# Kernel tuning notes

Measured on AMD Instinct MI355X. Metric: run time of the kernel, lower is better.

## Reference

```python
import jax, jax.numpy as jnp
import numpy as np

DIM = 64
POS_HID = 64
ATTN_HID = DIM * 4  # attn_mlp_hidden_mult = 4
B, N = 4, 512


def setup_inputs() -> dict:
    key = jax.random.key(0)
    ks = jax.random.split(key, 12)
    s = lambda fan_in: 1.0 / np.sqrt(fan_in)
    return {
        "x": jax.random.normal(ks[0], (B, N, DIM), dtype=jnp.float32),
        "pos": jax.random.normal(ks[1], (B, N, 3), dtype=jnp.float32),
        # to_qkv: Linear(dim, 3*dim, bias=False); stored as [in, out]
        "w_qkv": jax.random.uniform(ks[2], (DIM, 3 * DIM), jnp.float32, -s(DIM), s(DIM)),
        # pos_mlp: Linear(3, POS_HID) -> ReLU -> Linear(POS_HID, dim)
        "pos_w1": jax.random.uniform(ks[3], (3, POS_HID), jnp.float32, -s(3), s(3)),
        "pos_b1": jax.random.uniform(ks[4], (POS_HID,), jnp.float32, -s(3), s(3)),
        "pos_w2": jax.random.uniform(ks[5], (POS_HID, DIM), jnp.float32, -s(POS_HID), s(POS_HID)),
        "pos_b2": jax.random.uniform(ks[6], (DIM,), jnp.float32, -s(POS_HID), s(POS_HID)),
        # attn_mlp: Linear(dim, ATTN_HID) -> ReLU -> Linear(ATTN_HID, 1)
        "attn_w1": jax.random.uniform(ks[7], (DIM, ATTN_HID), jnp.float32, -s(DIM), s(DIM)),
        "attn_b1": jax.random.uniform(ks[8], (ATTN_HID,), jnp.float32, -s(DIM), s(DIM)),
        "attn_w2": jax.random.uniform(ks[9], (ATTN_HID, 1), jnp.float32, -s(ATTN_HID), s(ATTN_HID)),
        "attn_b2": jax.random.uniform(ks[10], (1,), jnp.float32, -s(ATTN_HID), s(ATTN_HID)),
    }


def reference(x, pos, w_qkv, pos_w1, pos_b1, pos_w2, pos_b2,
              attn_w1, attn_b1, attn_w2, attn_b2):
    # qkv projection: [b,n,3d] -> q,k,v each [b,n,d]
    qkv = x @ w_qkv
    q, k, v = jnp.split(qkv, 3, axis=-1)
    # pairwise relative positions: [b,n,n,3]
    rel_pos = pos[:, :, None, :] - pos[:, None, :, :]
    # pos_mlp: [b,n,n,d]
    rel_pos_emb = jax.nn.relu(rel_pos @ pos_w1 + pos_b1) @ pos_w2 + pos_b2
    # pairwise q-k differences: [b,n,n,d]
    qk_rel = q[:, :, None, :] - k[:, None, :, :]
    # attn_mlp -> scalar sim per pair: [b,n,n]
    h = qk_rel + rel_pos_emb
    sim = (jax.nn.relu(h @ attn_w1 + attn_b1) @ attn_w2 + attn_b2)[..., 0]
    attn = jax.nn.softmax(sim, axis=-1)
    # values augmented by positional embedding, weighted sum over j
    v_aug = v[:, None, :, :] + rel_pos_emb  # [b,n,n,d]
    agg = jnp.einsum('bij,bijd->bid', attn, v_aug)
    return agg
```

## Files before the change

### kernel.cpp

```cpp
#include <hip/hip_runtime.h>
#include <hip/hip_bf16.h>
#include <stdint.h>

#define DIM 64
#define TH  256
#define NN  512
#define IB  4

typedef __attribute__((ext_vector_type(8))) short bf16x8;
typedef __attribute__((ext_vector_type(4))) float f32x4;

__device__ __forceinline__ short f2bf(float f) {
    union { float f; uint32_t u; } v; v.f = f;
    uint32_t r = v.u + 0x7fffu + ((v.u >> 16) & 1u);
    return (short)(r >> 16);
}

__global__ void prep_all(const float* __restrict__ x, const float* __restrict__ w_qkv,
                         const float* __restrict__ attn_w1,
                         const float* __restrict__ pos_w2, const float* __restrict__ pos_b2,
                         const float* __restrict__ attn_b1,
                         float* __restrict__ V, float* __restrict__ QW1, short* __restrict__ Kneg,
                         short* __restrict__ Bg, float* __restrict__ cbg) {
    const int tid = threadIdx.x;
    if (blockIdx.x >= 256) {
        const int t = (blockIdx.x - 256) * 32 + (tid >> 3);
        const int h0 = (tid & 7) * 8;
        float m[8] = {};
        for (int d = 0; d < DIM; d++) {
            float wa1 = attn_w1[d * TH + t];
            #pragma unroll
            for (int hh = 0; hh < 8; hh++) m[hh] += pos_w2[(h0 + hh) * DIM + d] * wa1;
        }
        #pragma unroll
        for (int hh = 0; hh < 8; hh++) {
            Bg[t * 128 + h0 + hh] = f2bf(m[hh]);
            Bg[t * 128 + 64 + h0 + hh] = f2bf(attn_w1[(h0 + hh) * TH + t]);
        }
        if ((tid & 7) == 0) {
            float cb = attn_b1[t];
            for (int d = 0; d < DIM; d++) cb += pos_b2[d] * attn_w1[d * TH + t];
            cbg[t] = cb;
        }
        return;
    }
    const int b = blockIdx.x >> 6, j0 = (blockIdx.x & 63) * 8;
    __shared__ float xs[8][DIM], qs[8][DIM];
    #pragma unroll
    for (int p = 0; p < 2; p++) {
        int idx = tid + p * 256;
        xs[idx >> 6][idx & 63] = x[(size_t)(b * NN + j0) * DIM + idx];
    }
    __syncthreads();
    if (tid < 192) {
        float acc[8] = {};
        for (int e = 0; e < DIM; e++) {
            float wq = w_qkv[e * 192 + tid];
            #pragma unroll
            for (int jj = 0; jj < 8; jj++) acc[jj] += xs[jj][e] * wq;
        }
        #pragma unroll
        for (int jj = 0; jj < 8; jj++) {
            size_t row = (size_t)(b * NN + j0 + jj) * DIM;
            if (tid < 64)       qs[jj][tid] = acc[jj];
            else if (tid < 128) Kneg[row + (tid - 64)] = f2bf(-acc[jj]);
            else                V[row + (tid - 128)] = acc[jj];
        }
    }
    __syncthreads();
    float aq[8] = {};
    for (int d = 0; d < DIM; d++) {
        float w = attn_w1[d * TH + tid];
        #pragma unroll
        for (int jj = 0; jj < 8; jj++) aq[jj] += qs[jj][d] * w;
    }
    #pragma unroll
    for (int jj = 0; jj < 8; jj++)
        QW1[(size_t)(b * NN + j0 + jj) * TH + tid] = aq[jj];
}

__launch_bounds__(512, 2)
__global__ void ptl_main(const float* __restrict__ pos, const float* __restrict__ pos_w1,
                         const float* __restrict__ pos_b1, const float* __restrict__ pos_w2,
                         const float* __restrict__ pos_b2, const float* __restrict__ attn_w2,
                         const float* __restrict__ V, const float* __restrict__ QW1,
                         const short* __restrict__ Kneg, const short* __restrict__ Bg,
                         const float* __restrict__ cbg, float* __restrict__ out) {
    const int b = blockIdx.x >> 7, i0 = (blockIdx.x & 127) * IB;
    const int tid = threadIdx.x;
    const int wv = tid >> 6, lane = tid & 63;
    const int lhi = lane >> 4, llo = lane & 15;

    __shared__ __align__(16) short Blds[128 * 128];
    __shared__ float posl[NN][3];
    __shared__ float2 qwl[IB][TH];
    __shared__ float4 pw4[DIM];
    __shared__ float simbuf[IB][NN];
    __shared__ float aggw[8][IB][2][DIM];
    __shared__ float fin[IB][2][DIM];
    __shared__ float wred[2][IB][8];

    for (int idx = tid; idx < NN * 3; idx += 512)
        ((float*)posl)[idx] = pos[b * NN * 3 + idx];
    if (tid < TH) {
        float w2 = attn_w2[tid], cb = cbg[tid];
        #pragma unroll
        for (int ii = 0; ii < IB; ii++) {
            float2 q2; q2.x = QW1[(size_t)(b * NN + i0 + ii) * TH + tid] + cb; q2.y = w2;
            qwl[ii][tid] = q2;
        }
    }
    if (tid < DIM) {
        float4 w; w.x = pos_w1[tid]; w.y = pos_w1[DIM + tid];
        w.z = pos_w1[2 * DIM + tid]; w.w = pos_b1[tid];
        pw4[tid] = w;
    }
    bf16x8 knf[4][2];
    #pragma unroll
    for (int jt = 0; jt < 4; jt++) {
        size_t row = (size_t)(b * NN + wv * 64 + jt * 16 + llo) * DIM;
        knf[jt][0] = *(const bf16x8*)(Kneg + row + lhi * 8);
        knf[jt][1] = *(const bf16x8*)(Kneg + row + 32 + lhi * 8);
    }
    __syncthreads();

    const char* mb = (const char*)Blds + llo * 256;
    const int s0 = ((0  + lhi) ^ llo) << 4;
    const int s1 = ((4  + lhi) ^ llo) << 4;
    const int s2 = ((8  + lhi) ^ llo) << 4;
    const int s3 = ((12 + lhi) ^ llo) << 4;

    #pragma unroll 1
    for (int half = 0; half < 2; half++) {
        if (half) __syncthreads();
        for (int idx = tid; idx < 128 * 16; idx += 512) {
            int t = idx >> 4, s = idx & 15;
            *(uint4*)((char*)Blds + t * 256 + ((s ^ (t & 15)) << 4)) =
                *(const uint4*)((const char*)Bg + ((size_t)half * 2048 + idx) * 16);
        }
        __syncthreads();

        #pragma unroll 1
        for (int ii = 0; ii < IB; ii++) {
            const float pi0 = posl[i0 + ii][0], pi1 = posl[i0 + ii][1], pi2 = posl[i0 + ii][2];
            bf16x8 gfr[4][2];
            #pragma unroll
            for (int jt = 0; jt < 4; jt++) {
                const int jA = wv * 64 + jt * 16 + llo;
                const float r0 = pi0 - posl[jA][0], r1 = pi1 - posl[jA][1], r2 = pi2 - posl[jA][2];
                #pragma unroll
                for (int kk = 0; kk < 2; kk++) {
                    #pragma unroll
                    for (int e2 = 0; e2 < 4; e2++) {
                        float4 wA = pw4[kk * 32 + lhi * 8 + 2 * e2];
                        float4 wB = pw4[kk * 32 + lhi * 8 + 2 * e2 + 1];
                        float2 p2;
                        p2.x = fmaxf(r0 * wA.x + r1 * wA.y + r2 * wA.z + wA.w, 0.f);
                        p2.y = fmaxf(r0 * wB.x + r1 * wB.y + r2 * wB.z + wB.w, 0.f);
                        union { __hip_bfloat162 h2; uint32_t u; } cv;
                        cv.h2 = __float22bfloat162_rn(p2);
                        ((uint32_t*)&gfr[jt][kk])[e2] = cv.u;
                    }
                }
            }
            float sa[4][4] = {};
            #pragma unroll 4
            for (int tt = 0; tt < 8; tt++) {
                const int t = half * 128 + tt * 16 + llo;
                bf16x8 bf0 = *(const bf16x8*)(mb + tt * 4096 + s0);
                bf16x8 bf1 = *(const bf16x8*)(mb + tt * 4096 + s1);
                bf16x8 bf2 = *(const bf16x8*)(mb + tt * 4096 + s2);
                bf16x8 bf3 = *(const bf16x8*)(mb + tt * 4096 + s3);
                const float2 qw = qwl[ii][t];
                #pragma unroll
                for (int jt = 0; jt < 4; jt++) {
                    f32x4 acc = {0.f, 0.f, 0.f, 0.f};
                    acc = __builtin_amdgcn_mfma_f32_16x16x32_bf16(gfr[jt][0], bf0, acc, 0, 0, 0);
                    acc = __builtin_amdgcn_mfma_f32_16x16x32_bf16(gfr[jt][1], bf1, acc, 0, 0, 0);
                    acc = __builtin_amdgcn_mfma_f32_16x16x32_bf16(knf[jt][0], bf2, acc, 0, 0, 0);
                    acc = __builtin_amdgcn_mfma_f32_16x16x32_bf16(knf[jt][1], bf3, acc, 0, 0, 0);
                    #pragma unroll
                    for (int r = 0; r < 4; r++)
                        sa[jt][r] += fmaxf(acc[r] + qw.x, 0.f) * qw.y;
                }
            }
            #pragma unroll
            for (int jt = 0; jt < 4; jt++) {
                #pragma unroll
                for (int r = 0; r < 4; r++) {
                    float v = sa[jt][r];
                    v += __shfl_xor(v, 1); v += __shfl_xor(v, 2);
                    v += __shfl_xor(v, 4); v += __shfl_xor(v, 8);
                    if (llo == 0) {
                        const int j = wv * 64 + jt * 16 + lhi * 4 + r;
                        if (half == 0) simbuf[ii][j] = v;
                        else           simbuf[ii][j] += v;
                    }
                }
            }
        }
    }
    __syncthreads();

    float sv[IB];
    #pragma unroll
    for (int ii = 0; ii < IB; ii++) {
        float s = simbuf[ii][tid];
        sv[ii] = s;
        float mx = s;
        #pragma unroll
        for (int off = 1; off < 64; off <<= 1) mx = fmaxf(mx, __shfl_xor(mx, off));
        if (lane == 0) wred[0][ii][wv] = mx;
    }
    __syncthreads();
    float pv[IB];
    #pragma unroll
    for (int ii = 0; ii < IB; ii++) {
        float bm = wred[0][ii][0];
        #pragma unroll
        for (int w = 1; w < 8; w++) bm = fmaxf(bm, wred[0][ii][w]);
        float p = __expf(sv[ii] - bm);
        pv[ii] = p;
        float ps = p;
        #pragma unroll
        for (int off = 1; off < 64; off <<= 1) ps += __shfl_xor(ps, off);
        if (lane == 0) wred[1][ii][wv] = ps;
    }
    __syncthreads();
    #pragma unroll
    for (int ii = 0; ii < IB; ii++) {
        float den = 0.f;
        #pragma unroll
        for (int w = 0; w < 8; w++) den += wred[1][ii][w];
        simbuf[ii][tid] = pv[ii] / den;
    }
    __syncthreads();

    {
        const int d = lane;
        const float4 wd = pw4[d];
        float pia[IB][3];
        #pragma unroll
        for (int ii = 0; ii < IB; ii++) {
            pia[ii][0] = posl[i0 + ii][0]; pia[ii][1] = posl[i0 + ii][1]; pia[ii][2] = posl[i0 + ii][2];
        }
        float av[IB] = {}, ag[IB] = {};
        const float* vb = V + (size_t)(b * NN + wv * 64) * DIM + d;
        #pragma unroll 4
        for (int jj = 0; jj < 64; jj++) {
            const int j = wv * 64 + jj;
            const float vv = vb[jj * DIM];
            const float p0 = posl[j][0], p1 = posl[j][1], p2 = posl[j][2];
            #pragma unroll
            for (int ii = 0; ii < IB; ii++) {
                const float a = simbuf[ii][j];
                av[ii] += a * vv;
                float g = (pia[ii][0] - p0) * wd.x + (pia[ii][1] - p1) * wd.y +
                          (pia[ii][2] - p2) * wd.z + wd.w;
                ag[ii] += a * fmaxf(g, 0.f);
            }
        }
        #pragma unroll
        for (int ii = 0; ii < IB; ii++) {
            aggw[wv][ii][0][d] = av[ii];
            aggw[wv][ii][1][d] = ag[ii];
        }
    }
    __syncthreads();
    {
        const int ii = tid >> 7, pp = (tid >> 6) & 1, d2 = tid & 63;
        float s = 0.f;
        #pragma unroll
        for (int w = 0; w < 8; w++) s += aggw[w][ii][pp][d2];
        fin[ii][pp][d2] = s;
    }
    __syncthreads();
    if (tid < IB * DIM) {
        const int ii = tid >> 6, d2 = tid & 63;
        float o = fin[ii][0][d2] + pos_b2[d2];
        for (int h = 0; h < DIM; h++) o += fin[ii][1][h] * pos_w2[h * DIM + d2];
        out[(size_t)(b * NN + i0 + ii) * DIM + d2] = o;
    }
}

extern "C" void kernel_launch(void* const* d_in, const int* in_sizes, int n_in,
                              void* d_out, int out_size, void* d_ws, size_t ws_size,
                              hipStream_t stream) {
    const float* x       = (const float*)d_in[0];
    const float* pos     = (const float*)d_in[1];
    const float* w_qkv   = (const float*)d_in[2];
    const float* pos_w1  = (const float*)d_in[3];
    const float* pos_b1  = (const float*)d_in[4];
    const float* pos_w2  = (const float*)d_in[5];
    const float* pos_b2  = (const float*)d_in[6];
    const float* attn_w1 = (const float*)d_in[7];
    const float* attn_b1 = (const float*)d_in[8];
    const float* attn_w2 = (const float*)d_in[9];

    char* ws = (char*)d_ws;
    short* Bg   = (short*)(ws + 0);
    float* cbg  = (float*)(ws + 65536);
    float* Vw   = (float*)(ws + 66560);
    float* QW1  = (float*)(ws + 590848);
    short* Kneg = (short*)(ws + 2688000);

    float* outp = (float*)d_out;

    prep_all<<<264, 256, 0, stream>>>(x, w_qkv, attn_w1, pos_w2, pos_b2, attn_b1,
                                      Vw, QW1, Kneg, Bg, cbg);
    ptl_main<<<4 * (NN / IB), 512, 0, stream>>>(pos, pos_w1, pos_b1, pos_w2, pos_b2,
                                                attn_w2, Vw, QW1, Kneg, Bg, cbg, outp);
}
```

Measured before the change: 234.3 us.

## Use 1024-thread blocks with 8 query rows and full resident attn_w1 tile

Doubles the query rows per block to 8 and the block size to 1024 threads, so each wave handles 32 key columns instead of 64. The full 256-wide hidden weight tile is kept in LDS, loaded once, which removes the two-pass half loop and its extra barriers. Softmax and the aggregation are restructured for 16 waves, with the aggregation done in two groups of four rows. LDS use roughly doubles and the grid halves to 256 blocks, which may reduce occupancy or leave CUs idle.

```diff
diff --git a/kernel.cpp b/kernel.cpp
--- a/kernel.cpp
+++ b/kernel.cpp
@@ -5,7 +5,7 @@
 #define DIM 64
 #define TH  256
 #define NN  512
-#define IB  4
+#define IB  8
 
 typedef __attribute__((ext_vector_type(8))) short bf16x8;
 typedef __attribute__((ext_vector_type(4))) float f32x4;
@@ -79,46 +79,57 @@
         QW1[(size_t)(b * NN + j0 + jj) * TH + tid] = aq[jj];
 }
 
-__launch_bounds__(512, 2)
+__launch_bounds__(1024, 4)
 __global__ void ptl_main(const float* __restrict__ pos, const float* __restrict__ pos_w1,
                          const float* __restrict__ pos_b1, const float* __restrict__ pos_w2,
                          const float* __restrict__ pos_b2, const float* __restrict__ attn_w2,
                          const float* __restrict__ V, const float* __restrict__ QW1,
                          const short* __restrict__ Kneg, const short* __restrict__ Bg,
                          const float* __restrict__ cbg, float* __restrict__ out) {
-    const int b = blockIdx.x >> 7, i0 = (blockIdx.x & 127) * IB;
+    const int b = blockIdx.x >> 6, i0 = (blockIdx.x & 63) * IB;
     const int tid = threadIdx.x;
     const int wv = tid >> 6, lane = tid & 63;
     const int lhi = lane >> 4, llo = lane & 15;
 
-    __shared__ __align__(16) short Blds[128 * 128];
+    __shared__ __align__(16) short Blds[TH * 128];
     __shared__ float posl[NN][3];
     __shared__ float2 qwl[IB][TH];
     __shared__ float4 pw4[DIM];
     __shared__ float simbuf[IB][NN];
-    __shared__ float aggw[8][IB][2][DIM];
+    __shared__ float aggw[16][4][2][DIM];
     __shared__ float fin[IB][2][DIM];
     __shared__ float wred[2][IB][8];
 
-    for (int idx = tid; idx < NN * 3; idx += 512)
-        ((float*)posl)[idx] = pos[b * NN * 3 + idx];
-    if (tid < TH) {
-        float w2 = attn_w2[tid], cb = cbg[tid];
-        #pragma unroll
-        for (int ii = 0; ii < IB; ii++) {
-            float2 q2; q2.x = QW1[(size_t)(b * NN + i0 + ii) * TH + tid] + cb; q2.y = w2;
-            qwl[ii][tid] = q2;
-        }
+    #pragma unroll
+    for (int p = 0; p < 4; p++) {
+        int idx = tid + p * 1024;
+        int t = idx >> 4, s = idx & 15;
+        *(uint4*)((char*)Blds + t * 256 + ((s ^ (t & 15)) << 4)) =
+            *(const uint4*)((const char*)Bg + (size_t)idx * 16);
+    }
+    #pragma unroll
+    for (int p = 0; p < 2; p++) {
+        int idx = tid + p * 1024;
+        if (idx < NN * 3) ((float*)posl)[idx] = pos[b * NN * 3 + idx];
+    }
+    #pragma unroll
+    for (int p = 0; p < 2; p++) {
+        int idx = tid + p * 1024;
+        int ii = idx >> 8, t = idx & 255;
+        float2 q2;
+        q2.x = QW1[(size_t)(b * NN + i0 + ii) * TH + t] + cbg[t];
+        q2.y = attn_w2[t];
+        qwl[ii][t] = q2;
     }
     if (tid < DIM) {
         float4 w; w.x = pos_w1[tid]; w.y = pos_w1[DIM + tid];
         w.z = pos_w1[2 * DIM + tid]; w.w = pos_b1[tid];
         pw4[tid] = w;
     }
-    bf16x8 knf[4][2];
-    #pragma unroll
-    for (int jt = 0; jt < 4; jt++) {
-        size_t row = (size_t)(b * NN + wv * 64 + jt * 16 + llo) * DIM;
+    bf16x8 knf[2][2];
+    #pragma unroll
+    for (int jt = 0; jt < 2; jt++) {
+        size_t row = (size_t)(b * NN + wv * 32 + jt * 16 + llo) * DIM;
         knf[jt][0] = *(const bf16x8*)(Kneg + row + lhi * 8);
         knf[jt][1] = *(const bf16x8*)(Kneg + row + 32 + lhi * 8);
     }
@@ -131,148 +142,136 @@
     const int s3 = ((12 + lhi) ^ llo) << 4;
 
     #pragma unroll 1
-    for (int half = 0; half < 2; half++) {
-        if (half) __syncthreads();
-        for (int idx = tid; idx < 128 * 16; idx += 512) {
-            int t = idx >> 4, s = idx & 15;
-            *(uint4*)((char*)Blds + t * 256 + ((s ^ (t & 15)) << 4)) =
-                *(const uint4*)((const char*)Bg + ((size_t)half * 2048 + idx) * 16);
+    for (int ii = 0; ii < IB; ii++) {
+        const float pi0 = posl[i0 + ii][0], pi1 = posl[i0 + ii][1], pi2 = posl[i0 + ii][2];
+        bf16x8 gfr[2][2];
+        #pragma unroll
+        for (int jt = 0; jt < 2; jt++) {
+            const int jA = wv * 32 + jt * 16 + llo;
+            const float r0 = pi0 - posl[jA][0], r1 = pi1 - posl[jA][1], r2 = pi2 - posl[jA][2];
+            #pragma unroll
+            for (int kk = 0; kk < 2; kk++) {
+                #pragma unroll
+                for (int e2 = 0; e2 < 4; e2++) {
+                    float4 wA = pw4[kk * 32 + lhi * 8 + 2 * e2];
+                    float4 wB = pw4[kk * 32 + lhi * 8 + 2 * e2 + 1];
+                    float2 p2;
+                    p2.x = fmaxf(r0 * wA.x + r1 * wA.y + r2 * wA.z + wA.w, 0.f);
+                    p2.y = fmaxf(r0 * wB.x + r1 * wB.y + r2 * wB.z + wB.w, 0.f);
+                    union { __hip_bfloat162 h2; uint32_t u; } cv;
+                    cv.h2 = __float22bfloat162_rn(p2);
+                    ((uint32_t*)&gfr[jt][kk])[e2] = cv.u;
+                }
+            }
+        }
+        float sa[2][4] = {};
+        #pragma unroll 4
+        for (int tt = 0; tt < 16; tt++) {
+            const int t = tt * 16 + llo;
+            bf16x8 bf0 = *(const bf16x8*)(mb + tt * 4096 + s0);
+            bf16x8 bf1 = *(const bf16x8*)(mb + tt * 4096 + s1);
+            bf16x8 bf2 = *(const bf16x8*)(mb + tt * 4096 + s2);
+            bf16x8 bf3 = *(const bf16x8*)(mb + tt * 4096 + s3);
+            const float2 qw = qwl[ii][t];
+            #pragma unroll
+            for (int jt = 0; jt < 2; jt++) {
+                f32x4 acc = {0.f, 0.f, 0.f, 0.f};
+                acc = __builtin_amdgcn_mfma_f32_16x16x32_bf16(gfr[jt][0], bf0, acc, 0, 0, 0);
+                acc = __builtin_amdgcn_mfma_f32_16x16x32_bf16(gfr[jt][1], bf1, acc, 0, 0, 0);
+                acc = __builtin_amdgcn_mfma_f32_16x16x32_bf16(knf[jt][0], bf2, acc, 0, 0, 0);
+                acc = __builtin_amdgcn_mfma_f32_16x16x32_bf16(knf[jt][1], bf3, acc, 0, 0, 0);
+                #pragma unroll
+                for (int r = 0; r < 4; r++)
+                    sa[jt][r] += fmaxf(acc[r] + qw.x, 0.f) * qw.y;
+            }
+        }
+        #pragma unroll
+        for (int jt = 0; jt < 2; jt++) {
+            #pragma unroll
+            for (int r = 0; r < 4; r++) {
+                float v = sa[jt][r];
+                v += __shfl_xor(v, 1); v += __shfl_xor(v, 2);
+                v += __shfl_xor(v, 4); v += __shfl_xor(v, 8);
+                if (llo == 0) simbuf[ii][wv * 32 + jt * 16 + lhi * 4 + r] = v;
+            }
+        }
+    }
+    __syncthreads();
+
+    const int iig = wv >> 3, w8 = wv & 7, j = tid & 511;
+    float sv[4], pv[4];
+    #pragma unroll
+    for (int c = 0; c < 4; c++) {
+        const int ii = 2 * c + iig;
+        float s = simbuf[ii][j];
+        sv[c] = s;
+        float mx = s;
+        #pragma unroll
+        for (int off = 1; off < 64; off <<= 1) mx = fmaxf(mx, __shfl_xor(mx, off));
+        if (lane == 0) wred[0][ii][w8] = mx;
+    }
+    __syncthreads();
+    #pragma unroll
+    for (int c = 0; c < 4; c++) {
+        const int ii = 2 * c + iig;
+        float bm = wred[0][ii][0];
+        #pragma unroll
+        for (int w = 1; w < 8; w++) bm = fmaxf(bm, wred[0][ii][w]);
+        float p = __expf(sv[c] - bm);
+        pv[c] = p;
+        float ps = p;
+        #pragma unroll
+        for (int off = 1; off < 64; off <<= 1) ps += __shfl_xor(ps, off);
+        if (lane == 0) wred[1][ii][w8] = ps;
+    }
+    __syncthreads();
+    #pragma unroll
+    for (int c = 0; c < 4; c++) {
+        const int ii = 2 * c + iig;
+        float den = 0.f;
+        #pragma unroll
+        for (int w = 0; w < 8; w++) den += wred[1][ii][w];
+        simbuf[ii][j] = pv[c] / den;
+    }
+    __syncthreads();
+
+    #pragma unroll 1
+    for (int g = 0; g < 2; g++) {
+        if (g) __syncthreads();
+        {
+            const int d = lane;
+            const float4 wd = pw4[d];
+            float av[4] = {}, ag[4] = {};
+            const float* vb = V + (size_t)(b * NN + wv * 32) * DIM + d;
+            #pragma unroll 4
+            for (int jj = 0; jj < 32; jj++) {
+                const int jx = wv * 32 + jj;
+                const float vv = vb[jj * DIM];
+                const float p0 = posl[jx][0], p1 = posl[jx][1], p2 = posl[jx][2];
+                #pragma unroll
+                for (int c = 0; c < 4; c++) {
+                    const int ii = g * 4 + c;
+                    const float a = simbuf[ii][jx];
+                    av[c] += a * vv;
+                    float gg = (posl[i0 + ii][0] - p0) * wd.x + (posl[i0 + ii][1] - p1) * wd.y +
+                               (posl[i0 + ii][2] - p2) * wd.z + wd.w;
+                    ag[c] += a * fmaxf(gg, 0.f);
+                }
+            }
+            #pragma unroll
+            for (int c = 0; c < 4; c++) {
+                aggw[wv][c][0][d] = av[c];
+                aggw[wv][c][1][d] = ag[c];
+            }
         }
         __syncthreads();
-
-        #pragma unroll 1
-        for (int ii = 0; ii < IB; ii++) {
-            const float pi0 = posl[i0 + ii][0], pi1 = posl[i0 + ii][1], pi2 = posl[i0 + ii][2];
-            bf16x8 gfr[4][2];
-            #pragma unroll
-            for (int jt = 0; jt < 4; jt++) {
-                const int jA = wv * 64 + jt * 16 + llo;
-                const float r0 = pi0 - posl[jA][0], r1 = pi1 - posl[jA][1], r2 = pi2 - posl[jA][2];
-                #pragma unroll
-                for (int kk = 0; kk < 2; kk++) {
-                    #pragma unroll
-                    for (int e2 = 0; e2 < 4; e2++) {
-                        float4 wA = pw4[kk * 32 + lhi * 8 + 2 * e2];
-                        float4 wB = pw4[kk * 32 + lhi * 8 + 2 * e2 + 1];
-                        float2 p2;
-                        p2.x = fmaxf(r0 * wA.x + r1 * wA.y + r2 * wA.z + wA.w, 0.f);
-                        p2.y = fmaxf(r0 * wB.x + r1 * wB.y + r2 * wB.z + wB.w, 0.f);
-                        union { __hip_bfloat162 h2; uint32_t u; } cv;
-                        cv.h2 = __float22bfloat162_rn(p2);
-                        ((uint32_t*)&gfr[jt][kk])[e2] = cv.u;
-                    }
-                }
-            }
-            float sa[4][4] = {};
-            #pragma unroll 4
-            for (int tt = 0; tt < 8; tt++) {
-                const int t = half * 128 + tt * 16 + llo;
-                bf16x8 bf0 = *(const bf16x8*)(mb + tt * 4096 + s0);
-                bf16x8 bf1 = *(const bf16x8*)(mb + tt * 4096 + s1);
-                bf16x8 bf2 = *(const bf16x8*)(mb + tt * 4096 + s2);
-                bf16x8 bf3 = *(const bf16x8*)(mb + tt * 4096 + s3);
-                const float2 qw = qwl[ii][t];
-                #pragma unroll
-                for (int jt = 0; jt < 4; jt++) {
-                    f32x4 acc = {0.f, 0.f, 0.f, 0.f};
-                    acc = __builtin_amdgcn_mfma_f32_16x16x32_bf16(gfr[jt][0], bf0, acc, 0, 0, 0);
-                    acc = __builtin_amdgcn_mfma_f32_16x16x32_bf16(gfr[jt][1], bf1, acc, 0, 0, 0);
-                    acc = __builtin_amdgcn_mfma_f32_16x16x32_bf16(knf[jt][0], bf2, acc, 0, 0, 0);
-                    acc = __builtin_amdgcn_mfma_f32_16x16x32_bf16(knf[jt][1], bf3, acc, 0, 0, 0);
-                    #pragma unroll
-                    for (int r = 0; r < 4; r++)
-                        sa[jt][r] += fmaxf(acc[r] + qw.x, 0.f) * qw.y;
-                }
-            }
-            #pragma unroll
-            for (int jt = 0; jt < 4; jt++) {
-                #pragma unroll
-                for (int r = 0; r < 4; r++) {
-                    float v = sa[jt][r];
-                    v += __shfl_xor(v, 1); v += __shfl_xor(v, 2);
-                    v += __shfl_xor(v, 4); v += __shfl_xor(v, 8);
-                    if (llo == 0) {
-                        const int j = wv * 64 + jt * 16 + lhi * 4 + r;
-                        if (half == 0) simbuf[ii][j] = v;
-                        else           simbuf[ii][j] += v;
-                    }
-                }
-            }
-        }
-    }
-    __syncthreads();
-
-    float sv[IB];
-    #pragma unroll
-    for (int ii = 0; ii < IB; ii++) {
-        float s = simbuf[ii][tid];
-        sv[ii] = s;
-        float mx = s;
-        #pragma unroll
-        for (int off = 1; off < 64; off <<= 1) mx = fmaxf(mx, __shfl_xor(mx, off));
-        if (lane == 0) wred[0][ii][wv] = mx;
-    }
-    __syncthreads();
-    float pv[IB];
-    #pragma unroll
-    for (int ii = 0; ii < IB; ii++) {
-        float bm = wred[0][ii][0];
-        #pragma unroll
-        for (int w = 1; w < 8; w++) bm = fmaxf(bm, wred[0][ii][w]);
-        float p = __expf(sv[ii] - bm);
-        pv[ii] = p;
-        float ps = p;
-        #pragma unroll
-        for (int off = 1; off < 64; off <<= 1) ps += __shfl_xor(ps, off);
-        if (lane == 0) wred[1][ii][wv] = ps;
-    }
-    __syncthreads();
-    #pragma unroll
-    for (int ii = 0; ii < IB; ii++) {
-        float den = 0.f;
-        #pragma unroll
-        for (int w = 0; w < 8; w++) den += wred[1][ii][w];
-        simbuf[ii][tid] = pv[ii] / den;
-    }
-    __syncthreads();
-
-    {
-        const int d = lane;
-        const float4 wd = pw4[d];
-        float pia[IB][3];
-        #pragma unroll
-        for (int ii = 0; ii < IB; ii++) {
-            pia[ii][0] = posl[i0 + ii][0]; pia[ii][1] = posl[i0 + ii][1]; pia[ii][2] = posl[i0 + ii][2];
-        }
-        float av[IB] = {}, ag[IB] = {};
-        const float* vb = V + (size_t)(b * NN + wv * 64) * DIM + d;
-        #pragma unroll 4
-        for (int jj = 0; jj < 64; jj++) {
-            const int j = wv * 64 + jj;
-            const float vv = vb[jj * DIM];
-            const float p0 = posl[j][0], p1 = posl[j][1], p2 = posl[j][2];
-            #pragma unroll
-            for (int ii = 0; ii < IB; ii++) {
-                const float a = simbuf[ii][j];
-                av[ii] += a * vv;
-                float g = (pia[ii][0] - p0) * wd.x + (pia[ii][1] - p1) * wd.y +
-                          (pia[ii][2] - p2) * wd.z + wd.w;
-                ag[ii] += a * fmaxf(g, 0.f);
-            }
-        }
-        #pragma unroll
-        for (int ii = 0; ii < IB; ii++) {
-            aggw[wv][ii][0][d] = av[ii];
-            aggw[wv][ii][1][d] = ag[ii];
-        }
-    }
-    __syncthreads();
-    {
-        const int ii = tid >> 7, pp = (tid >> 6) & 1, d2 = tid & 63;
-        float s = 0.f;
-        #pragma unroll
-        for (int w = 0; w < 8; w++) s += aggw[w][ii][pp][d2];
-        fin[ii][pp][d2] = s;
+        if (tid < 512) {
+            const int c = tid >> 7, pp = (tid >> 6) & 1, d2 = tid & 63;
+            float s = 0.f;
+            #pragma unroll
+            for (int w = 0; w < 16; w++) s += aggw[w][c][pp][d2];
+            fin[g * 4 + c][pp][d2] = s;
+        }
     }
     __syncthreads();
     if (tid < IB * DIM) {
@@ -308,6 +307,6 @@
 
     prep_all<<<264, 256, 0, stream>>>(x, w_qkv, attn_w1, pos_w2, pos_b2, attn_b1,
                                       Vw, QW1, Kneg, Bg, cbg);
-    ptl_main<<<4 * (NN / IB), 512, 0, stream>>>(pos, pos_w1, pos_b1, pos_w2, pos_b2,
-                                                attn_w2, Vw, QW1, Kneg, Bg, cbg, outp);
+    ptl_main<<<4 * (NN / IB), 1024, 0, stream>>>(pos, pos_w1, pos_b1, pos_w2, pos_b2,
+                                                 attn_w2, Vw, QW1, Kneg, Bg, cbg, outp);
 }
```

Measured after the change: 208.3 us. 1.13x faster.

## Split j-tiles into two passes to cut registers; parallelize weight prep

Applied to the files above, without the earlier changes.

The main kernel now processes the 64 j-columns per wave as two 32-column passes, loading K fragments per pass. This halves the live fragment and accumulator arrays, which is meant to lower register pressure and raise occupancy, at the cost of recomputing the pos-MLP fragments' loop overhead and reloading B tiles' use per pass. The q·W1 bias is now folded into the MFMA accumulator's initial value. The weight-fusion part of prep is re-parallelized across 64 blocks of 4 columns with shared-memory staging and float4 loads, replacing the serial per-thread dot products.

```diff
diff --git a/kernel.cpp b/kernel.cpp
--- a/kernel.cpp
+++ b/kernel.cpp
@@ -24,23 +24,25 @@
                          short* __restrict__ Bg, float* __restrict__ cbg) {
     const int tid = threadIdx.x;
     if (blockIdx.x >= 256) {
-        const int t = (blockIdx.x - 256) * 32 + (tid >> 3);
-        const int h0 = (tid & 7) * 8;
-        float m[8] = {};
-        for (int d = 0; d < DIM; d++) {
-            float wa1 = attn_w1[d * TH + t];
-            #pragma unroll
-            for (int hh = 0; hh < 8; hh++) m[hh] += pos_w2[(h0 + hh) * DIM + d] * wa1;
-        }
-        #pragma unroll
-        for (int hh = 0; hh < 8; hh++) {
-            Bg[t * 128 + h0 + hh] = f2bf(m[hh]);
-            Bg[t * 128 + 64 + h0 + hh] = f2bf(attn_w1[(h0 + hh) * TH + t]);
-        }
-        if ((tid & 7) == 0) {
-            float cb = attn_b1[t];
-            for (int d = 0; d < DIM; d++) cb += pos_b2[d] * attn_w1[d * TH + t];
-            cbg[t] = cb;
+        __shared__ float colW[64][4];
+        const int t0 = (blockIdx.x - 256) * 4;
+        const int dw = tid >> 2, c = tid & 3;
+        colW[dw][c] = attn_w1[dw * TH + t0 + c];
+        __syncthreads();
+        const int h = tid >> 2;
+        float m = 0.f;
+        #pragma unroll 4
+        for (int dd = 0; dd < DIM; dd += 4) {
+            float4 pw = *(const float4*)&pos_w2[h * DIM + dd];
+            m += pw.x * colW[dd][c] + pw.y * colW[dd + 1][c] +
+                 pw.z * colW[dd + 2][c] + pw.w * colW[dd + 3][c];
+        }
+        Bg[(t0 + c) * 128 + h] = f2bf(m);
+        Bg[(t0 + c) * 128 + 64 + h] = f2bf(attn_w1[h * TH + t0 + c]);
+        if (h == 0) {
+            float cb = attn_b1[t0 + c];
+            for (int dd = 0; dd < DIM; dd++) cb += pos_b2[dd] * colW[dd][c];
+            cbg[t0 + c] = cb;
         }
         return;
     }
@@ -115,14 +117,6 @@
         w.z = pos_w1[2 * DIM + tid]; w.w = pos_b1[tid];
         pw4[tid] = w;
     }
-    bf16x8 knf[4][2];
-    #pragma unroll
-    for (int jt = 0; jt < 4; jt++) {
-        size_t row = (size_t)(b * NN + wv * 64 + jt * 16 + llo) * DIM;
-        knf[jt][0] = *(const bf16x8*)(Kneg + row + lhi * 8);
-        knf[jt][1] = *(const bf16x8*)(Kneg + row + 32 + lhi * 8);
-    }
-    __syncthreads();
 
     const char* mb = (const char*)Blds + llo * 256;
     const int s0 = ((0  + lhi) ^ llo) << 4;
@@ -132,7 +126,7 @@
 
     #pragma unroll 1
     for (int half = 0; half < 2; half++) {
-        if (half) __syncthreads();
+        __syncthreads();
         for (int idx = tid; idx < 128 * 16; idx += 512) {
             int t = idx >> 4, s = idx & 15;
             *(uint4*)((char*)Blds + t * 256 + ((s ^ (t & 15)) << 4)) =
@@ -141,60 +135,71 @@
         __syncthreads();
 
         #pragma unroll 1
-        for (int ii = 0; ii < IB; ii++) {
-            const float pi0 = posl[i0 + ii][0], pi1 = posl[i0 + ii][1], pi2 = posl[i0 + ii][2];
-            bf16x8 gfr[4][2];
+        for (int p = 0; p < 2; p++) {
+            const int jbase = p * 256 + wv * 32;
+            bf16x8 knf[2][2];
             #pragma unroll
-            for (int jt = 0; jt < 4; jt++) {
-                const int jA = wv * 64 + jt * 16 + llo;
-                const float r0 = pi0 - posl[jA][0], r1 = pi1 - posl[jA][1], r2 = pi2 - posl[jA][2];
+            for (int jt = 0; jt < 2; jt++) {
+                size_t row = (size_t)(b * NN + jbase + jt * 16 + llo) * DIM;
+                knf[jt][0] = *(const bf16x8*)(Kneg + row + lhi * 8);
+                knf[jt][1] = *(const bf16x8*)(Kneg + row + 32 + lhi * 8);
+            }
+            #pragma unroll 1
+            for (int ii = 0; ii < IB; ii++) {
+                const float pi0 = posl[i0 + ii][0], pi1 = posl[i0 + ii][1], pi2 = posl[i0 + ii][2];
+                bf16x8 gfr[2][2];
                 #pragma unroll
-                for (int kk = 0; kk < 2; kk++) {
+                for (int jt = 0; jt < 2; jt++) {
+                    const int jA = jbase + jt * 16 + llo;
+                    const float r0 = pi0 - posl[jA][0], r1 = pi1 - posl[jA][1], r2 = pi2 - posl[jA][2];
                     #pragma unroll
-                    for (int e2 = 0; e2 < 4; e2++) {
-                        float4 wA = pw4[kk * 32 + lhi * 8 + 2 * e2];
-                        float4 wB = pw4[kk * 32 + lhi * 8 + 2 * e2 + 1];
-                        float2 p2;
-                        p2.x = fmaxf(r0 * wA.x + r1 * wA.y + r2 * wA.z + wA.w, 0.f);
-                        p2.y = fmaxf(r0 * wB.x + r1 * wB.y + r2 * wB.z + wB.w, 0.f);
-                        union { __hip_bfloat162 h2; uint32_t u; } cv;
-                        cv.h2 = __float22bfloat162_rn(p2);
-                        ((uint32_t*)&gfr[jt][kk])[e2] = cv.u;
+                    for (int kk = 0; kk < 2; kk++) {
+                        #pragma unroll
+                        for (int e2 = 0; e2 < 4; e2++) {
+                            float4 wA = pw4[kk * 32 + lhi * 8 + 2 * e2];
+                            float4 wB = pw4[kk * 32 + lhi * 8 + 2 * e2 + 1];
+                            float2 p2;
+                            p2.x = fmaxf(r0 * wA.x + r1 * wA.y + r2 * wA.z + wA.w, 0.f);
+                            p2.y = fmaxf(r0 * wB.x + r1 * wB.y + r2 * wB.z + wB.w, 0.f);
+                            union { __hip_bfloat162 h2; uint32_t u; } cv;
+                            cv.h2 = __float22bfloat162_rn(p2);
+                            ((uint32_t*)&gfr[jt][kk])[e2] = cv.u;
+                        }
                     }
                 }
-            }
-            float sa[4][4] = {};
-            #pragma unroll 4
-            for (int tt = 0; tt < 8; tt++) {
-                const int t = half * 128 + tt * 16 + llo;
-                bf16x8 bf0 = *(const bf16x8*)(mb + tt * 4096 + s0);
-                bf16x8 bf1 = *(const bf16x8*)(mb + tt * 4096 + s1);
-                bf16x8 bf2 = *(const bf16x8*)(mb + tt * 4096 + s2);
-                bf16x8 bf3 = *(const bf16x8*)(mb + tt * 4096 + s3);
-                const float2 qw = qwl[ii][t];
+                float sa[2][4] = {};
+                #pragma unroll 4
+                for (int tt = 0; tt < 8; tt++) {
+                    const int t = half * 128 + tt * 16 + llo;
+                    bf16x8 bf0 = *(const bf16x8*)(mb + tt * 4096 + s0);
+                    bf16x8 bf1 = *(const bf16x8*)(mb + tt * 4096 + s1);
+                    bf16x8 bf2 = *(const bf16x8*)(mb + tt * 4096 + s2);
+                    bf16x8 bf3 = *(const bf16x8*)(mb + tt * 4096 + s3);
+                    const float2 qw = qwl[ii][t];
+                    #pragma unroll
+                    for (int jt = 0; jt < 2; jt++) {
+                        f32x4 acc = {qw.x, qw.x, qw.x, qw.x};
+                        acc = __builtin_amdgcn_mfma_f32_16x16x32_bf16(gfr[jt][0], bf0, acc, 0, 0, 0);
+                        acc = __builtin_amdgcn_mfma_f32_16x16x32_bf16(gfr[jt][1], bf1, acc, 0, 0, 0);
+                        acc = __builtin_amdgcn_mfma_f32_16x16x32_bf16(knf[jt][0], bf2, acc, 0, 0, 0);
+                        acc = __builtin_amdgcn_mfma_f32_16x16x32_bf16(knf[jt][1], bf3, acc, 0, 0, 0);
+                        #pragma unroll
+                        for (int r = 0; r < 4; r++)
+                            sa[jt][r] += fmaxf(acc[r], 0.f) * qw.y;
+                    }
+                }
                 #pragma unroll
-                for (int jt = 0; jt < 4; jt++) {
-                    f32x4 acc = {0.f, 0.f, 0.f, 0.f};
-                    acc = __builtin_amdgcn_mfma_f32_16x16x32_bf16(gfr[jt][0], bf0, acc, 0, 0, 0);
-                    acc = __builtin_amdgcn_mfma_f32_16x16x32_bf16(gfr[jt][1], bf1, acc, 0, 0, 0);
-                    acc = __builtin_amdgcn_mfma_f32_16x16x32_bf16(knf[jt][0], bf2, acc, 0, 0, 0);
-                    acc = __builtin_amdgcn_mfma_f32_16x16x32_bf16(knf[jt][1], bf3, acc, 0, 0, 0);
+                for (int jt = 0; jt < 2; jt++) {
                     #pragma unroll
-                    for (int r = 0; r < 4; r++)
-                        sa[jt][r] += fmaxf(acc[r] + qw.x, 0.f) * qw.y;
-                }
-            }
-            #pragma unroll
-            for (int jt = 0; jt < 4; jt++) {
-                #pragma unroll
-                for (int r = 0; r < 4; r++) {
-                    float v = sa[jt][r];
-                    v += __shfl_xor(v, 1); v += __shfl_xor(v, 2);
-                    v += __shfl_xor(v, 4); v += __shfl_xor(v, 8);
-                    if (llo == 0) {
-                        const int j = wv * 64 + jt * 16 + lhi * 4 + r;
-                        if (half == 0) simbuf[ii][j] = v;
-                        else           simbuf[ii][j] += v;
+                    for (int r = 0; r < 4; r++) {
+                        float v = sa[jt][r];
+                        v += __shfl_xor(v, 1); v += __shfl_xor(v, 2);
+                        v += __shfl_xor(v, 4); v += __shfl_xor(v, 8);
+                        if (llo == 0) {
+                            const int j = jbase + jt * 16 + lhi * 4 + r;
+                            if (half == 0) simbuf[ii][j] = v;
+                            else           simbuf[ii][j] += v;
+                        }
                     }
                 }
             }
@@ -306,7 +311,7 @@
 
     float* outp = (float*)d_out;
 
-    prep_all<<<264, 256, 0, stream>>>(x, w_qkv, attn_w1, pos_w2, pos_b2, attn_b1,
+    prep_all<<<320, 256, 0, stream>>>(x, w_qkv, attn_w1, pos_w2, pos_b2, attn_b1,
                                       Vw, QW1, Kneg, Bg, cbg);
     ptl_main<<<4 * (NN / IB), 512, 0, stream>>>(pos, pos_w1, pos_b1, pos_w2, pos_b2,
                                                 attn_w2, Vw, QW1, Kneg, Bg, cbg, outp);
```

Measured after the change: 223.9 us. -4.5%, faster.
